# Performance work log

Measured on AMD Instinct MI355X. Metric: run time of the kernel, lower is better.

## Reference

```python
import jax, jax.numpy as jnp
import numpy as np

N0 = 50000
N1 = 50000
F = 512
H = 64
C = 20
E = 1_600_000


def setup_inputs() -> dict:
    key = jax.random.key(0)
    ks = jax.random.split(key, 20)
    inp = {
        'feat_0': jax.random.normal(ks[0], (N0, F), jnp.float32),
        'feat_1': jax.random.normal(ks[1], (N1, F), jnp.float32),
        'W1_00': jax.random.normal(ks[2], (F, H), jnp.float32) * 0.05,
        'W1_01': jax.random.normal(ks[3], (F, H), jnp.float32) * 0.05,
        'W1_10': jax.random.normal(ks[4], (F, H), jnp.float32) * 0.05,
        'W1_11': jax.random.normal(ks[5], (F, H), jnp.float32) * 0.05,
        'W2_00': jax.random.normal(ks[6], (H, C), jnp.float32) * 0.05,
        'W2_01': jax.random.normal(ks[7], (H, C), jnp.float32) * 0.05,
        'W2_10': jax.random.normal(ks[8], (H, C), jnp.float32) * 0.05,
        'W2_11': jax.random.normal(ks[9], (H, C), jnp.float32) * 0.05,
        'vals_00': jax.random.uniform(ks[10], (E,), jnp.float32),
        'vals_01': jax.random.uniform(ks[11], (E,), jnp.float32),
        'vals_10': jax.random.uniform(ks[12], (E,), jnp.float32),
        'vals_11': jax.random.uniform(ks[13], (E,), jnp.float32),
        'edge_idx_00': jax.random.randint(ks[14], (2, E), 0, N0, jnp.int32),
        'edge_idx_01': jax.random.randint(ks[15], (2, E), 0, N0, jnp.int32),
        'edge_idx_10': jax.random.randint(ks[16], (2, E), 0, N1, jnp.int32),
        'edge_idx_11': jax.random.randint(ks[17], (2, E), 0, N1, jnp.int32),
    }
    return inp


def _spmm(edge_idx, vals, x, n_out):
    # A @ x where A is COO: edge_idx[0]=row (dst type i), edge_idx[1]=col (src type j)
    msg = vals[:, None] * x[edge_idx[1]]            # [E, D] gather
    return jax.ops.segment_sum(msg, edge_idx[0], num_segments=n_out)


def reference(feat_0, feat_1, W1_00, W1_01, W1_10, W1_11,
              W2_00, W2_01, W2_10, W2_11,
              vals_00, vals_01, vals_10, vals_11,
              edge_idx_00, edge_idx_01, edge_idx_10, edge_idx_11):
    # layer 1: hidden1[i] = relu(sum_j A_ij @ (feat_j @ W1_ij))
    h0 = jax.nn.relu(_spmm(edge_idx_00, vals_00, feat_0 @ W1_00, N0)
                     + _spmm(edge_idx_01, vals_01, feat_1 @ W1_01, N0))
    h1 = jax.nn.relu(_spmm(edge_idx_10, vals_10, feat_0 @ W1_10, N1)
                     + _spmm(edge_idx_11, vals_11, feat_1 @ W1_11, N1))
    # layer 2: embeddings[i] = sum_j A_ij @ (hidden1[j] @ W2_ij)
    emb0 = (_spmm(edge_idx_00, vals_00, h0 @ W2_00, N0)
            + _spmm(edge_idx_01, vals_01, h1 @ W2_01, N0))
    emb1 = (_spmm(edge_idx_10, vals_10, h0 @ W2_10, N1)
            + _spmm(edge_idx_11, vals_11, h1 @ W2_11, N1))
    return jnp.stack([emb0, emb1])  # [2, N, C]
```

## Files before the change

kernel.cpp:

```cpp
#include <hip/hip_runtime.h>
#include <hip/hip_bf16.h>

#define NNODES 50000
#define FDIM   512
#define HDIM   64
#define CDIM   20
#define NEDGE  1600000
#define NB     392
#define SEB    16384
#define SBLK   98

typedef unsigned short ushort_t;
typedef __attribute__((ext_vector_type(8))) short bf16x8;
typedef __attribute__((ext_vector_type(4))) float f32x4;

static __device__ __forceinline__ ushort_t f2bf(float f) {
    __hip_bfloat16 h = __float2bfloat16(f);
    return *reinterpret_cast<ushort_t*>(&h);
}
static __device__ __forceinline__ bf16x8 pack_bf8(float4 v0, float4 v1) {
    bf16x8 r;
    r[0] = (short)f2bf(v0.x); r[1] = (short)f2bf(v0.y);
    r[2] = (short)f2bf(v0.z); r[3] = (short)f2bf(v0.w);
    r[4] = (short)f2bf(v1.x); r[5] = (short)f2bf(v1.y);
    r[6] = (short)f2bf(v1.z); r[7] = (short)f2bf(v1.w);
    return r;
}

__global__ __launch_bounds__(256) void wt_kernel(
    const float* __restrict__ W00, const float* __restrict__ W10,
    const float* __restrict__ W01, const float* __restrict__ W11,
    ushort_t* __restrict__ Wt0, ushort_t* __restrict__ Wt1)
{
    const int c    = blockIdx.x;
    const int type = blockIdx.y;
    const float* W;
    if (type == 0) W = (c < 64) ? W00 : W10;
    else           W = (c < 64) ? W01 : W11;
    const int cc = c & 63;
    ushort_t* Wt = type ? Wt1 : Wt0;
    #pragma unroll
    for (int kb = 0; kb < 2; ++kb) {
        int k = kb * 256 + threadIdx.x;
        Wt[c * 512 + k] = f2bf(W[k * 64 + cc]);
    }
}

__global__ __launch_bounds__(256) void proj1_kernel(
    const float* __restrict__ f0, const float* __restrict__ f1,
    const ushort_t* __restrict__ Wt0, const ushort_t* __restrict__ Wt1,
    ushort_t* __restrict__ X0, ushort_t* __restrict__ X1)
{
    const float* feat; const ushort_t* Wt; ushort_t* X;
    if (blockIdx.y == 0) { feat = f0; Wt = Wt0; X = X0; }
    else                 { feat = f1; Wt = Wt1; X = X1; }

    __shared__ ushort_t Bs[128 * 512];

    const int t    = threadIdx.x;
    const int wave = t >> 6;
    const int lane = t & 63;
    const int lrow = lane & 15;
    const int kgrp = lane >> 4;

    #pragma unroll 8
    for (int idx = t; idx < 128 * 64; idx += 256) {
        int c = idx >> 6;
        int s = idx & 63;
        bf16x8 v = *(const bf16x8*)(Wt + c * 512 + s * 8);
        *(bf16x8*)&Bs[c * 512 + ((s ^ (c & 7)) * 8)] = v;
    }
    __syncthreads();

    const int rowStrip = blockIdx.x * 128 + wave * 32;

    f32x4 acc[2][8];
    #pragma unroll
    for (int rt = 0; rt < 2; ++rt)
        #pragma unroll
        for (int ct = 0; ct < 8; ++ct)
            acc[rt][ct] = (f32x4){0.f, 0.f, 0.f, 0.f};

    long rA0 = rowStrip + lrow;       if (rA0 > NNODES - 1) rA0 = NNODES - 1;
    long rA1 = rowStrip + 16 + lrow;  if (rA1 > NNODES - 1) rA1 = NNODES - 1;
    const float* pA0 = feat + rA0 * FDIM + kgrp * 8;
    const float* pA1 = feat + rA1 * FDIM + kgrp * 8;

    #pragma unroll 4
    for (int k0 = 0; k0 < FDIM; k0 += 32) {
        float4 v0 = *(const float4*)(pA0 + k0);
        float4 v1 = *(const float4*)(pA0 + k0 + 4);
        float4 w0 = *(const float4*)(pA1 + k0);
        float4 w1 = *(const float4*)(pA1 + k0 + 4);
        bf16x8 a0 = pack_bf8(v0, v1);
        bf16x8 a1 = pack_bf8(w0, w1);
        const int sbase = (k0 >> 3) + kgrp;
        #pragma unroll
        for (int ct = 0; ct < 8; ++ct) {
            const int c = ct * 16 + lrow;
            bf16x8 b = *(const bf16x8*)&Bs[c * 512 + ((sbase ^ (c & 7)) * 8)];
            acc[0][ct] = __builtin_amdgcn_mfma_f32_16x16x32_bf16(a0, b, acc[0][ct], 0, 0, 0);
            acc[1][ct] = __builtin_amdgcn_mfma_f32_16x16x32_bf16(a1, b, acc[1][ct], 0, 0, 0);
        }
    }

    #pragma unroll
    for (int rt = 0; rt < 2; ++rt) {
        #pragma unroll
        for (int r = 0; r < 4; ++r) {
            int row = rowStrip + rt * 16 + kgrp * 4 + r;
            if (row < NNODES) {
                #pragma unroll
                for (int ct = 0; ct < 8; ++ct)
                    X[(long)row * 128 + ct * 16 + lrow] = f2bf(acc[rt][ct][r]);
            }
        }
    }
}

__global__ __launch_bounds__(512) void bhist_kernel(
    const int* __restrict__ e00, const int* __restrict__ e01,
    const int* __restrict__ e10, const int* __restrict__ e11,
    int* __restrict__ bcnt, int* __restrict__ blkcnt)
{
    int r = blockIdx.y;
    const int* e = (r == 0) ? e00 : (r == 1) ? e01 : (r == 2) ? e10 : e11;
    __shared__ int lc[NB];
    const int t = threadIdx.x;
    if (t < NB) lc[t] = 0;
    __syncthreads();
    const int e0 = blockIdx.x * SEB;
    #pragma unroll 4
    for (int k = 0; k < 32; ++k) {
        int i = e0 + t + k * 512;
        if (i < NEDGE) atomicAdd(&lc[e[i] >> 7], 1);
    }
    __syncthreads();
    if (t < NB) {
        int c = lc[t];
        blkcnt[(r * NB + t) * SBLK + blockIdx.x] = c;
        if (c) atomicAdd(&bcnt[r * NB + t], c);
    }
}

__global__ __launch_bounds__(512) void bscan_kernel(
    const int* __restrict__ bcnt, int* __restrict__ boff)
{
    int r = blockIdx.x;
    __shared__ int s[512];
    const int t = threadIdx.x;
    int v = (t < NB) ? bcnt[r * NB + t] : 0;
    s[t] = v;
    __syncthreads();
    #pragma unroll
    for (int d = 1; d < 512; d <<= 1) {
        int add = (t >= d) ? s[t - d] : 0;
        __syncthreads();
        s[t] += add;
        __syncthreads();
    }
    if (t < NB) boff[r * NB + t] = s[t] - v;
}

__global__ __launch_bounds__(128) void blkscan_kernel(
    const int* __restrict__ boff, const int* __restrict__ blkcnt,
    int* __restrict__ blkbase)
{
    const int b = blockIdx.x;
    const int r = blockIdx.y;
    const int t = threadIdx.x;
    __shared__ int s[128];
    int v = (t < SBLK) ? blkcnt[(r * NB + b) * SBLK + t] : 0;
    s[t] = v;
    __syncthreads();
    #pragma unroll
    for (int d = 1; d < 128; d <<= 1) {
        int add = (t >= d) ? s[t - d] : 0;
        __syncthreads();
        s[t] += add;
        __syncthreads();
    }
    if (t < SBLK) blkbase[(r * NB + b) * SBLK + t] = boff[r * NB + b] + s[t] - v;
}

__global__ __launch_bounds__(512) void bscatter_kernel(
    const int* __restrict__ e00, const int* __restrict__ e01,
    const int* __restrict__ e10, const int* __restrict__ e11,
    const float* __restrict__ v00, const float* __restrict__ v01,
    const float* __restrict__ v10, const float* __restrict__ v11,
    const int* __restrict__ blkbase, uint2* __restrict__ staged)
{
    int r = blockIdx.y;
    const int* e; const float* v;
    if      (r == 0) { e = e00; v = v00; }
    else if (r == 1) { e = e01; v = v01; }
    else if (r == 2) { e = e10; v = v10; }
    else             { e = e11; v = v11; }

    __shared__ int lcur[NB];
    const int t = threadIdx.x;
    if (t < NB) lcur[t] = blkbase[(r * NB + t) * SBLK + blockIdx.x];
    __syncthreads();
    const int e0 = blockIdx.x * SEB;
    uint2* st = staged + (long)r * NEDGE;
    #pragma unroll 4
    for (int k = 0; k < 32; ++k) {
        int i = e0 + t + k * 512;
        if (i < NEDGE) {
            int dst = e[i];
            int src = e[NEDGE + i];
            float val = v[i];
            int pos = atomicAdd(&lcur[dst >> 7], 1);
            st[pos] = make_uint2(((unsigned)dst << 16) | (unsigned)src, __float_as_uint(val));
        }
    }
}

__global__ __launch_bounds__(256) void bfinal_kernel(
    const int* __restrict__ boff, const int* __restrict__ bcnt,
    const uint2* __restrict__ staged,
    int* __restrict__ rowptr, unsigned* __restrict__ edata)
{
    const int b = blockIdx.x;
    const int r = blockIdx.y;
    const int t = threadIdx.x;
    const int s0  = boff[r * NB + b];
    const int cnt = bcnt[r * NB + b];
    const int e1  = s0 + cnt;
    const uint2* st = staged + (long)r * NEDGE;
    unsigned* ed = edata + (long)r * NEDGE;

    __shared__ int ncnt[128];
    __shared__ int sc[128];
    __shared__ int lcur[128];
    if (t < 128) ncnt[t] = 0;
    __syncthreads();
    for (int p = s0 + t; p < e1; p += 256)
        atomicAdd(&ncnt[(st[p].x >> 16) & 127], 1);
    __syncthreads();
    if (t < 128) sc[t] = ncnt[t];
    __syncthreads();
    #pragma unroll
    for (int d = 1; d < 128; d <<= 1) {
        int add = (t >= d && t < 128) ? sc[t - d] : 0;
        __syncthreads();
        if (t < 128) sc[t] += add;
        __syncthreads();
    }
    if (t < 128) {
        int excl = sc[t] - ncnt[t];
        int node = b * 128 + t;
        if (node <= NNODES) rowptr[r * (NNODES + 1) + node] = s0 + excl;
        lcur[t] = s0 + excl;
    }
    __syncthreads();
    for (int p = s0 + t; p < e1; p += 256) {
        uint2 w = st[p];
        int pos = atomicAdd(&lcur[(w.x >> 16) & 127], 1);
        ed[pos] = ((w.x & 0xffffu) << 16) | (unsigned)f2bf(__uint_as_float(w.y));
    }
}

#define G1_PAIR(uA, uB, ax, ay)                                              \
    {                                                                        \
        unsigned u_ = half ? (uB) : (uA);                                    \
        float vv_ = __uint_as_float((u_ & 0xffffu) << 16);                   \
        unsigned x_ = *(const unsigned*)&X[(u_ >> 16) * 128u + colOff + hl * 2]; \
        ax = fmaf(vv_, __uint_as_float(x_ << 16), ax);                       \
        ay = fmaf(vv_, __uint_as_float(x_ & 0xffff0000u), ay);               \
    }

__global__ __launch_bounds__(256) void gather1_kernel(
    const int* __restrict__ rowptr, const unsigned* __restrict__ edata,
    const ushort_t* __restrict__ X0, const ushort_t* __restrict__ X1,
    float* __restrict__ h0, float* __restrict__ h1)
{
    const int i    = blockIdx.y;
    const int lane = threadIdx.x & 63;
    const int node = __builtin_amdgcn_readfirstlane(blockIdx.x * 4 + (threadIdx.x >> 6));
    const int half = lane >> 5;
    const int hl   = lane & 31;
    const unsigned colOff = i * 64;

    float a0 = 0.f, a1 = 0.f, b0 = 0.f, b1 = 0.f;
    float c0 = 0.f, c1 = 0.f, d0 = 0.f, d1 = 0.f;

    #pragma unroll
    for (int j = 0; j < 2; ++j) {
        const int r = i * 2 + j;
        const int* rp = rowptr + r * (NNODES + 1);
        const unsigned* ed = edata + (long)r * NEDGE;
        const ushort_t* X = j ? X1 : X0;
        int s = __builtin_amdgcn_readfirstlane(rp[node]);
        int e = __builtin_amdgcn_readfirstlane(rp[node + 1]);
        int p = s;
        for (; p + 8 <= e; p += 8) {
            unsigned u0 = ed[p],     u1 = ed[p + 1], u2 = ed[p + 2], u3 = ed[p + 3];
            unsigned u4 = ed[p + 4], u5 = ed[p + 5], u6 = ed[p + 6], u7 = ed[p + 7];
            G1_PAIR(u0, u1, a0, a1);
            G1_PAIR(u2, u3, b0, b1);
            G1_PAIR(u4, u5, c0, c1);
            G1_PAIR(u6, u7, d0, d1);
        }
        if (p < e) {
            int rem = e - p;
            unsigned u0 = ed[p],     u1 = ed[p + 1], u2 = ed[p + 2], u3 = ed[p + 3];
            unsigned u4 = ed[p + 4], u5 = ed[p + 5], u6 = ed[p + 6], u7 = ed[p + 7];
            unsigned base = u0 & 0xffff0000u;
            unsigned z1 = (rem > 1) ? u1 : base;
            unsigned z2 = (rem > 2) ? u2 : base;
            unsigned z3 = (rem > 3) ? u3 : base;
            unsigned z4 = (rem > 4) ? u4 : base;
            unsigned z5 = (rem > 5) ? u5 : base;
            unsigned z6 = (rem > 6) ? u6 : base;
            unsigned z7 = (rem > 7) ? u7 : base;
            G1_PAIR(u0, z1, a0, a1);
            G1_PAIR(z2, z3, b0, b1);
            G1_PAIR(z4, z5, c0, c1);
            G1_PAIR(z6, z7, d0, d1);
        }
    }
    float r0 = (a0 + b0) + (c0 + d0);
    float r1 = (a1 + b1) + (c1 + d1);
    r0 += __shfl_xor(r0, 32);
    r1 += __shfl_xor(r1, 32);
    float* h = i ? h1 : h0;
    if (lane < 32)
        *(float2*)&h[node * 64 + hl * 2] = make_float2(r0, r1);
}

__global__ __launch_bounds__(256) void proj2_kernel(
    const float* __restrict__ hacc, const float* __restrict__ W2a,
    const float* __restrict__ W2b, ushort_t* __restrict__ y)
{
    __shared__ float hs[32][65];
    __shared__ float ws[64][40];
    const int t = threadIdx.x;

    for (int p = t; p < 64 * 40; p += 256) {
        int k = p / 40, c = p % 40;
        ws[k][c] = (c < 20) ? W2a[k * 20 + c] : W2b[k * 20 + (c - 20)];
    }
    const int nodeBase = blockIdx.x * 32;
    for (int p = t; p < 32 * 64; p += 256) {
        int n = p >> 6, k = p & 63;
        float hv = 0.f;
        if (nodeBase + n < NNODES) hv = hacc[(long)(nodeBase + n) * HDIM + k];
        hs[n][k] = fmaxf(hv, 0.f);
    }
    __syncthreads();

    const int n  = t >> 3;
    const int cg = (t & 7) * 5;
    float acc[5] = {0.f, 0.f, 0.f, 0.f, 0.f};
    #pragma unroll 16
    for (int k = 0; k < 64; ++k) {
        float hv = hs[n][k];
        #pragma unroll
        for (int j = 0; j < 5; ++j) acc[j] = fmaf(hv, ws[k][cg + j], acc[j]);
    }
    if (nodeBase + n < NNODES) {
        #pragma unroll
        for (int j = 0; j < 5; ++j)
            y[(long)(nodeBase + n) * 40 + cg + j] = f2bf(acc[j]);
    }
}

#define G2_SIX(U0,U1,U2,U3,U4,U5, ax, ay)                                    \
    {                                                                        \
        unsigned u_ = (g==0)?(U0):(g==1)?(U1):(g==2)?(U2):(g==3)?(U3):(g==4)?(U4):(U5); \
        float vv_ = __uint_as_float((u_ & 0xffffu) << 16);                   \
        unsigned y_ = *(const unsigned*)&y[(u_ >> 16) * 40u + colOff + c * 2]; \
        ax = fmaf(vv_, __uint_as_float(y_ << 16), ax);                       \
        ay = fmaf(vv_, __uint_as_float(y_ & 0xffff0000u), ay);               \
    }

__global__ __launch_bounds__(256) void gather2_kernel(
    const int* __restrict__ rowptr, const unsigned* __restrict__ edata,
    const ushort_t* __restrict__ y0, const ushort_t* __restrict__ y1,
    float* __restrict__ out)
{
    const int i    = blockIdx.y;
    const int lane = threadIdx.x & 63;
    const int node = __builtin_amdgcn_readfirstlane(blockIdx.x * 4 + (threadIdx.x >> 6));
    const int g = lane / 10;
    const int c = lane % 10;
    const unsigned colOff = i * 20;

    float accA0 = 0.f, accA1 = 0.f, accB0 = 0.f, accB1 = 0.f;

    #pragma unroll
    for (int j = 0; j < 2; ++j) {
        const int r = i * 2 + j;
        const int* rp = rowptr + r * (NNODES + 1);
        const unsigned* ed = edata + (long)r * NEDGE;
        const ushort_t* y = j ? y1 : y0;
        int s = __builtin_amdgcn_readfirstlane(rp[node]);
        int e = __builtin_amdgcn_readfirstlane(rp[node + 1]);
        int p = s;
        for (; p + 12 <= e; p += 12) {
            unsigned u0 = ed[p],     u1 = ed[p + 1],  u2 = ed[p + 2];
            unsigned u3 = ed[p + 3], u4 = ed[p + 4],  u5 = ed[p + 5];
            unsigned x0 = ed[p + 6], x1 = ed[p + 7],  x2 = ed[p + 8];
            unsigned x3 = ed[p + 9], x4 = ed[p + 10], x5 = ed[p + 11];
            G2_SIX(u0, u1, u2, u3, u4, u5, accA0, accA1);
            G2_SIX(x0, x1, x2, x3, x4, x5, accB0, accB1);
        }
        for (; p + 6 <= e; p += 6) {
            unsigned u0 = ed[p],     u1 = ed[p + 1], u2 = ed[p + 2];
            unsigned u3 = ed[p + 3], u4 = ed[p + 4], u5 = ed[p + 5];
            G2_SIX(u0, u1, u2, u3, u4, u5, accA0, accA1);
        }
        if (p < e) {
            int rem = e - p;
            unsigned u0 = ed[p],     u1 = ed[p + 1], u2 = ed[p + 2];
            unsigned u3 = ed[p + 3], u4 = ed[p + 4];
            unsigned base = u0 & 0xffff0000u;
            unsigned z1 = (rem > 1) ? u1 : base;
            unsigned z2 = (rem > 2) ? u2 : base;
            unsigned z3 = (rem > 3) ? u3 : base;
            unsigned z4 = (rem > 4) ? u4 : base;
            G2_SIX(u0, z1, z2, z3, z4, base, accA0, accA1);
        }
    }
    float u0 = (accA0 + accB0);
    float u1 = (accA1 + accB1);
    u0 += __shfl(u0, lane + 30);
    u1 += __shfl(u1, lane + 30);
    float q0 = u0 + __shfl(u0, lane + 10) + __shfl(u0, lane + 20);
    float q1 = u1 + __shfl(u1, lane + 10) + __shfl(u1, lane + 20);
    if (lane < 10)
        *(float2*)&out[i * (NNODES * CDIM) + node * CDIM + c * 2] = make_float2(q0, q1);
}

extern "C" void kernel_launch(void* const* d_in, const int* in_sizes, int n_in,
                              void* d_out, int out_size, void* d_ws, size_t ws_size,
                              hipStream_t stream) {
    const float* feat0 = (const float*)d_in[0];
    const float* feat1 = (const float*)d_in[1];
    const float* W1_00 = (const float*)d_in[2];
    const float* W1_01 = (const float*)d_in[3];
    const float* W1_10 = (const float*)d_in[4];
    const float* W1_11 = (const float*)d_in[5];
    const float* W2_00 = (const float*)d_in[6];
    const float* W2_01 = (const float*)d_in[7];
    const float* W2_10 = (const float*)d_in[8];
    const float* W2_11 = (const float*)d_in[9];
    const float* v00 = (const float*)d_in[10];
    const float* v01 = (const float*)d_in[11];
    const float* v10 = (const float*)d_in[12];
    const float* v11 = (const float*)d_in[13];
    const int* e00 = (const int*)d_in[14];
    const int* e01 = (const int*)d_in[15];
    const int* e10 = (const int*)d_in[16];
    const int* e11 = (const int*)d_in[17];

    unsigned* w = (unsigned*)d_ws;
    uint2*    staged  = (uint2*)w;
    ushort_t* X0      = (ushort_t*)w;
    ushort_t* X1      = (ushort_t*)(w + 3200000);
    ushort_t* y0      = (ushort_t*)(w + 6400000);
    ushort_t* y1      = (ushort_t*)(w + 7400000);
    unsigned* edata   = (unsigned*)(w + 12800000);
    float*    h0      = (float*)(w + 19200000);
    float*    h1      = (float*)(w + 22400000);
    int*      rowptr  = (int*)(w + 25600000);
    int*      bcnt    = (int*)(w + 25800004);
    int*      boff    = (int*)(w + 25801572);
    int*      blkcnt  = (int*)(w + 25803140);
    int*      blkbase = (int*)(w + 25956804);
    ushort_t* Wt0     = (ushort_t*)(w + 26110468);
    ushort_t* Wt1     = (ushort_t*)(w + 26143236);
    float*    out     = (float*)d_out;

    wt_kernel<<<dim3(128, 2), 256, 0, stream>>>(W1_00, W1_10, W1_01, W1_11, Wt0, Wt1);

    hipMemsetAsync(bcnt, 0, 4ull * NB * sizeof(int), stream);
    bhist_kernel<<<dim3(SBLK, 4), 512, 0, stream>>>(e00, e01, e10, e11, bcnt, blkcnt);
    bscan_kernel<<<4, 512, 0, stream>>>(bcnt, boff);
    blkscan_kernel<<<dim3(NB, 4), 128, 0, stream>>>(boff, blkcnt, blkbase);
    bscatter_kernel<<<dim3(SBLK, 4), 512, 0, stream>>>(
        e00, e01, e10, e11, v00, v01, v10, v11, blkbase, staged);
    bfinal_kernel<<<dim3(391, 4), 256, 0, stream>>>(boff, bcnt, staged, rowptr, edata);

    dim3 g1((NNODES + 127) / 128, 2);
    proj1_kernel<<<g1, 256, 0, stream>>>(feat0, feat1, Wt0, Wt1, X0, X1);

    gather1_kernel<<<dim3((NNODES + 3) / 4, 2), 256, 0, stream>>>(rowptr, edata, X0, X1, h0, h1);

    proj2_kernel<<<(NNODES + 31) / 32, 256, 0, stream>>>(h0, W2_00, W2_10, y0);
    proj2_kernel<<<(NNODES + 31) / 32, 256, 0, stream>>>(h1, W2_01, W2_11, y1);

    gather2_kernel<<<dim3((NNODES + 3) / 4, 2), 256, 0, stream>>>(rowptr, edata, y0, y1, out);
}
```

Baseline: 488.3 us.

## Bucket edges in LDS before writing contiguous staged runs in scatter

The bucket-scatter kernel now does a local prefix scan of per-bucket counts and sorts each block's edges into shared memory by destination bucket. Each wavefront then writes every bucket's run to the staged array contiguously, instead of each thread storing to a scattered global position. The goal is coalesced global stores and fewer random writes. In exchange it adds a 64 KB shared buffer that lowers occupancy, an extra scan, a re-read of src and val, and a packed entry that now carries only the low 7 bits of dst.

```diff
diff --git a/kernel.cpp b/kernel.cpp
--- a/kernel.cpp
+++ b/kernel.cpp
@@ -188,7 +188,8 @@
     const int* __restrict__ e10, const int* __restrict__ e11,
     const float* __restrict__ v00, const float* __restrict__ v01,
     const float* __restrict__ v10, const float* __restrict__ v11,
-    const int* __restrict__ blkbase, uint2* __restrict__ staged)
+    const int* __restrict__ blkcnt, const int* __restrict__ blkbase,
+    uint2* __restrict__ staged)
 {
     int r = blockIdx.y;
     const int* e; const float* v;
@@ -197,21 +198,61 @@
     else if (r == 2) { e = e10; v = v10; }
     else             { e = e11; v = v11; }
 
+    __shared__ unsigned ent[SEB];
+    __shared__ int s[512];
+    __shared__ int lpre[NB + 1];
     __shared__ int lcur[NB];
-    const int t = threadIdx.x;
-    if (t < NB) lcur[t] = blkbase[(r * NB + t) * SBLK + blockIdx.x];
-    __syncthreads();
-    const int e0 = blockIdx.x * SEB;
-    uint2* st = staged + (long)r * NEDGE;
+    __shared__ int gbase[NB];
+
+    const int t   = threadIdx.x;
+    const int blk = blockIdx.x;
+    const int e0  = blk * SEB;
+
+    int myc = (t < NB) ? blkcnt[(r * NB + t) * SBLK + blk] : 0;
+    s[t] = myc;
+    __syncthreads();
+    #pragma unroll
+    for (int d = 1; d < 512; d <<= 1) {
+        int add = (t >= d) ? s[t - d] : 0;
+        __syncthreads();
+        s[t] += add;
+        __syncthreads();
+    }
+    if (t < NB) {
+        int excl = s[t] - myc;
+        lpre[t] = excl;
+        lcur[t] = excl;
+        gbase[t] = blkbase[(r * NB + t) * SBLK + blk];
+    }
+    if (t == 511) lpre[NB] = s[511];
+    __syncthreads();
+
     #pragma unroll 4
     for (int k = 0; k < 32; ++k) {
         int i = e0 + t + k * 512;
         if (i < NEDGE) {
             int dst = e[i];
-            int src = e[NEDGE + i];
-            float val = v[i];
             int pos = atomicAdd(&lcur[dst >> 7], 1);
-            st[pos] = make_uint2(((unsigned)dst << 16) | (unsigned)src, __float_as_uint(val));
+            ent[pos] = ((unsigned)(dst & 127) << 14) | (unsigned)(i - e0);
+        }
+    }
+    __syncthreads();
+
+    const int wv   = t >> 6;
+    const int lane = t & 63;
+    uint2* st = staged + (long)r * NEDGE;
+    for (int b = wv; b < NB; b += 8) {
+        int ps = __builtin_amdgcn_readfirstlane(lpre[b]);
+        int pe = __builtin_amdgcn_readfirstlane(lpre[b + 1]);
+        int gb = __builtin_amdgcn_readfirstlane(gbase[b]);
+        for (int q = ps + lane; q < pe; q += 64) {
+            unsigned en = ent[q];
+            int idx = en & 0x3fff;
+            unsigned dl7 = (en >> 14) & 127u;
+            int gi = e0 + idx;
+            unsigned src = (unsigned)e[NEDGE + gi];
+            float val = v[gi];
+            st[gb + (q - ps)] = make_uint2((dl7 << 16) | src, __float_as_uint(val));
         }
     }
 }
@@ -480,7 +521,7 @@
     bscan_kernel<<<4, 512, 0, stream>>>(bcnt, boff);
     blkscan_kernel<<<dim3(NB, 4), 128, 0, stream>>>(boff, blkcnt, blkbase);
     bscatter_kernel<<<dim3(SBLK, 4), 512, 0, stream>>>(
-        e00, e01, e10, e11, v00, v01, v10, v11, blkbase, staged);
+        e00, e01, e10, e11, v00, v01, v10, v11, blkcnt, blkbase, staged);
     bfinal_kernel<<<dim3(391, 4), 256, 0, stream>>>(boff, bcnt, staged, rowptr, edata);
 
     dim3 g1((NNODES + 127) / 128, 2);
```

Result: no change. 493.8 us (+1.1%).
